# Kernel tuning notes

Measured on AMD Instinct MI355X. Metric: run time of the kernel, lower is better.

The kernel has to match this reference:

```python
import jax, jax.numpy as jnp
import numpy as np

K = 32  # neighbors per sampled point
EPS = 1e-5

def _layernorm(h, g, b):
    mu = jnp.mean(h, axis=-1, keepdims=True)
    var = jnp.mean((h - mu) ** 2, axis=-1, keepdims=True)
    return (h - mu) * jax.lax.rsqrt(var + EPS) * g + b


def setup_inputs() -> dict:
    key = jax.random.key(0)
    ks = jax.random.split(key, 20)
    N, M, D_IN, D_T = 32768, 4096, 64, 128
    s = lambda k, *sh: jax.random.normal(k, sh, dtype=jnp.float32) * 0.05
    inp = {
        "x": jax.random.normal(ks[0], (N, D_IN), dtype=jnp.float32),
        "pos": jax.random.normal(ks[1], (N, 3), dtype=jnp.float32),
        "idx": jax.random.randint(ks[2], (M,), 0, N, dtype=jnp.int32),
        "batch": jnp.zeros((N,), dtype=jnp.int32),
        # PointNetConv MLP [67 -> 128 -> 256] (ReLU after first layer only)
        "W1": s(ks[3], D_IN + 3, 128), "b1": jnp.zeros((128,), jnp.float32),
        "W2": s(ks[4], 128, 256),     "b2": jnp.zeros((256,), jnp.float32),
        # feature_reduction Linear(256, 128)
        "Wr": s(ks[5], 256, D_T), "br": jnp.zeros((D_T,), jnp.float32),
        # MultiheadAttention(128, 4)
        "in_proj_w": s(ks[6], D_T, 3 * D_T), "in_proj_b": jnp.zeros((3 * D_T,), jnp.float32),
        "out_proj_w": s(ks[7], D_T, D_T),    "out_proj_b": jnp.zeros((D_T,), jnp.float32),
        # transformer MLP [128 -> 256 -> 128]
        "Wm1": s(ks[8], D_T, 2 * D_T), "bm1": jnp.zeros((2 * D_T,), jnp.float32),
        "Wm2": s(ks[9], 2 * D_T, D_T), "bm2": jnp.zeros((D_T,), jnp.float32),
        # layer norms
        "g1": jnp.ones((D_T,), jnp.float32), "beta1": jnp.zeros((D_T,), jnp.float32),
        "g2": jnp.ones((D_T,), jnp.float32), "beta2": jnp.zeros((D_T,), jnp.float32),
    }
    return inp


def _forward(x, pos, idx, batch, W1, b1, W2, b2, Wr, br,
             in_proj_w, in_proj_b, out_proj_w, out_proj_b,
             Wm1, bm1, Wm2, bm2, g1, beta1, g2, beta2):
    q_pos = pos[idx]                                    # [M,3]
    # KNN: k nearest source points for each sampled (dst) point
    d2 = (jnp.sum(q_pos ** 2, -1, keepdims=True)
          - 2.0 * (q_pos @ pos.T)
          + jnp.sum(pos ** 2, -1)[None, :])             # [M,N]
    _, col = jax.lax.top_k(-d2, K)                      # [M,K] source indices
    # PointNetConv message: nn([x_j, pos_j - pos_i]), max-aggregate per dst
    x_j = x[col]                                        # [M,K,64]
    rel = pos[col] - q_pos[:, None, :]                  # [M,K,3]
    feat = jnp.concatenate([x_j, rel], axis=-1)         # [M,K,67]
    h = jax.nn.relu(feat @ W1 + b1) @ W2 + b2           # [M,K,256]
    agg = jnp.max(h, axis=1)                            # [M,256]
    xt = agg @ Wr + br                                  # [M,128]
    # TransformerBlock: x.view(M,1,128) -> MHA over seq len M, batch 1
    M, D = xt.shape
    H = 4
    Dh = D // H
    qkv = xt @ in_proj_w + in_proj_b                    # [M,3D]
    qh, kh, vh = [t.reshape(M, H, Dh) for t in jnp.split(qkv, 3, axis=-1)]
    scores = jnp.einsum('qhd,khd->hqk', qh, kh) / np.sqrt(Dh)
    attn = jax.nn.softmax(scores, axis=-1)
    att = jnp.einsum('hqk,khd->qhd', attn, vh).reshape(M, D)
    att = att @ out_proj_w + out_proj_b
    xt = _layernorm(xt + att, g1, beta1)
    mlp = jax.nn.relu(xt @ Wm1 + bm1) @ Wm2 + bm2
    xt = _layernorm(xt + mlp, g2, beta2)
    return xt, q_pos, batch[idx]


def reference(x, pos, idx, batch, W1, b1, W2, b2, Wr, br,
              in_proj_w, in_proj_b, out_proj_w, out_proj_b,
              Wm1, bm1, Wm2, bm2, g1, beta1, g2, beta2):
    return _forward(x, pos, idx, batch, W1, b1, W2, b2, Wr, br,
                    in_proj_w, in_proj_b, out_proj_w, out_proj_b,
                    Wm1, bm1, Wm2, bm2, g1, beta1, g2, beta2)
```

## Files before the change

kernel.cpp:

```cpp
#include <hip/hip_runtime.h>
#include <hip/hip_bf16.h>

#define DEV static __device__ __forceinline__

typedef __attribute__((ext_vector_type(8))) short          s16x8;
typedef __attribute__((ext_vector_type(8))) unsigned short u16x8;
typedef __attribute__((ext_vector_type(4))) float          f32x4;
typedef __attribute__((ext_vector_type(4))) unsigned int   u32x4;

#define MFMA16(A,B,C) __builtin_amdgcn_mfma_f32_16x16x32_bf16((A),(B),(C),0,0,0)

DEV unsigned short f2bf(float f) {
  unsigned int u = __builtin_bit_cast(unsigned int, f);
  u += 0x7fffu + ((u >> 16) & 1u);
  return (unsigned short)(u >> 16);
}

#define QSCL 0.25503562201f

#define GRID_LO  (-5.0f)
#define GRID_IH  (3.2f)

DEV int cellc(float v) {
  int c = (int)floorf((v - GRID_LO) * GRID_IH);
  return min(31, max(0, c));
}

constexpr size_t OFF_POS4  = 0;
constexpr size_t OFF_COL   = 524288;
constexpr size_t OFF_W1T   = 1048576;
constexpr size_t OFF_W2T   = OFF_W1T  + 24576;
constexpr size_t OFF_WRT   = OFF_W2T  + 65536;
constexpr size_t OFF_WQKVT = OFF_WRT  + 65536;
constexpr size_t OFF_WOUTT = OFF_WQKVT+ 98304;
constexpr size_t OFF_WM1T  = OFF_WOUTT+ 32768;
constexpr size_t OFF_WM2T  = OFF_WM1T + 65536;
constexpr size_t OFF_H     = OFF_WM2T + 65536;
constexpr size_t OFF_SPOS    = OFF_H;
constexpr size_t OFF_CELLCNT = OFF_H + 524288;
constexpr size_t OFF_CELLDSC = OFF_H + 655360;
constexpr size_t OFF_FILL    = OFF_H + 917504;
constexpr size_t OFF_PO      = OFF_H;
constexpr size_t OFF_PL      = OFF_H + 16777216;
constexpr size_t OFF_AGG   = OFF_H    + 33554432;
constexpr size_t OFF_XT0   = OFF_AGG  + 4194304;
constexpr size_t OFF_QKV   = OFF_XT0  + 2097152;
constexpr size_t OFF_ATT   = OFF_QKV  + 6291456;
constexpr size_t OFF_PRE   = OFF_ATT  + 2097152;
constexpr size_t OFF_XT1   = OFF_PRE  + 2097152;
constexpr size_t OFF_MLP1  = OFF_XT1  + 2097152;
constexpr size_t OFF_SBIAS = OFF_MLP1 + 4194304;

__global__ __launch_bounds__(256) void zero_k(int* __restrict__ p) {
  p[blockIdx.x * 256 + threadIdx.x] = 0;
}

__global__ __launch_bounds__(256) void prep_k(
    const float* __restrict__ pos, const float* __restrict__ W1,
    const float* __restrict__ W2, const float* __restrict__ Wr,
    const float* __restrict__ ipw, const float* __restrict__ ipb,
    const float* __restrict__ opw,
    const float* __restrict__ Wm1, const float* __restrict__ Wm2,
    float4* __restrict__ pos4, unsigned short* __restrict__ w1t,
    unsigned short* __restrict__ w2t, unsigned short* __restrict__ wrt,
    unsigned short* __restrict__ wqkvt, unsigned short* __restrict__ woutt,
    unsigned short* __restrict__ wm1t, unsigned short* __restrict__ wm2t,
    int* __restrict__ cellcnt, float* __restrict__ sbias) {
  int T = blockIdx.x * 256 + threadIdx.x;
  if (T < 32768) {
    float px = pos[T*3], py = pos[T*3+1], pz = pos[T*3+2];
    pos4[T] = make_float4(px, py, pz, 0.f);
    int cid = (cellc(pz)*32 + cellc(py))*32 + cellc(px);
    atomicAdd(&cellcnt[cid], 1);
    return;
  }
  T -= 32768;
  if (T < 128*96)  { int n=T/96,  k=T%96;  w1t[T]  = f2bf(k < 67 ? W1[k*128+n] : 0.f); return; }
  T -= 128*96;
  if (T < 256*128) { int n=T/128, k=T%128; w2t[T]  = f2bf(W2[k*256+n]);  return; }
  T -= 256*128;
  if (T < 128*256) { int n=T/256, k=T%256; wrt[T]  = f2bf(Wr[k*128+n]);  return; }
  T -= 128*256;
  if (T < 384*128) { int n=T/128, k=T%128;
                     float v = ipw[k*384+n];
                     if (n < 128) v *= QSCL;
                     wqkvt[T]= f2bf(v); return; }
  T -= 384*128;
  if (T < 128*128) { int n=T/128, k=T%128; woutt[T]= f2bf(opw[k*128+n]); return; }
  T -= 128*128;
  if (T < 256*128) { int n=T/128, k=T%128; wm1t[T] = f2bf(Wm1[k*256+n]); return; }
  T -= 256*128;
  if (T < 128*256) { int n=T/256, k=T%256; wm2t[T] = f2bf(Wm2[k*128+n]); return; }
  T -= 128*256;
  if (T < 384) { sbias[T] = ipb[T] * (T < 128 ? QSCL : 1.f); return; }
}

__global__ __launch_bounds__(1024) void prefix_k(const int* __restrict__ cnt,
                                                 int2* __restrict__ desc,
                                                 int* __restrict__ fill) {
  __shared__ int wsum[16];
  const int tid = threadIdx.x, lane = tid & 63, w = tid >> 6;
  int loc[32]; int s = 0;
  #pragma unroll
  for (int i = 0; i < 32; ++i) { loc[i] = cnt[tid*32 + i]; s += loc[i]; }
  int sc = s;
  #pragma unroll
  for (int off = 1; off < 64; off <<= 1) {
    int v = __shfl_up(sc, off);
    if (lane >= off) sc += v;
  }
  if (lane == 63) wsum[w] = sc;
  __syncthreads();
  if (tid == 0) {
    int run = 0;
    #pragma unroll
    for (int i = 0; i < 16; ++i) { int v = wsum[i]; wsum[i] = run; run += v; }
  }
  __syncthreads();
  int base = wsum[w] + (sc - s);
  #pragma unroll
  for (int i = 0; i < 32; ++i) {
    int c = tid*32 + i;
    desc[c] = make_int2(base, loc[i]);
    fill[c] = base;
    base += loc[i];
  }
}

__global__ __launch_bounds__(256) void scatter_k(const float4* __restrict__ pos4,
                                                 int* __restrict__ fill,
                                                 float4* __restrict__ spos) {
  int T = blockIdx.x * 256 + threadIdx.x;
  float4 p = pos4[T];
  int cid = (cellc(p.z)*32 + cellc(p.y))*32 + cellc(p.x);
  int slot = atomicAdd(&fill[cid], 1);
  spos[slot] = make_float4(p.x, p.y, p.z, __int_as_float(T));
}

#define KNN_CAP  320
#define KNN_TRIG 192
#define KNN_KEEP 33
#define KNN_INF  3e37f

__global__ __launch_bounds__(256) void knn_k(
    const float4* __restrict__ spos, const int2* __restrict__ desc,
    const float4* __restrict__ pos4, const int* __restrict__ idx,
    int* __restrict__ col,
    float* __restrict__ outqpos, float* __restrict__ outbatch) {
  __shared__ float bufd[4][KNN_CAP];
  __shared__ int   bufi[4][KNN_CAP];
  __shared__ int   shist[4][64];
  __shared__ int2  segs[4][128];
  const int tid = threadIdx.x, lane = tid & 63, w = tid >> 6;
  const unsigned long long ltmask = (1ull << lane) - 1ull;

  const int q = blockIdx.x * 4 + w;
  const int iq = idx[q];
  const float4 qp = pos4[iq];
  const float qx = qp.x, qy = qp.y, qz = qp.z;
  const int cx0 = cellc(qx), cy0 = cellc(qy), cz0 = cellc(qz);

  float t = KNN_INF;
  int cnt = 0;

  auto compact = [&]() {
    int c_ = min(cnt, KNN_CAP);
    float vd[5]; int vi[5], bs[5]; bool okv[5];
    float dmax = 1e-30f;
    #pragma unroll
    for (int s = 0; s < 5; ++s) {
      int o2 = s*64 + lane;
      okv[s] = o2 < c_;
      vd[s] = okv[s] ? bufd[w][o2] : 0.f;
      vi[s] = okv[s] ? bufi[w][o2] : 0;
      dmax = fmaxf(dmax, vd[s]);
    }
    #pragma unroll
    for (int off = 1; off < 64; off <<= 1) dmax = fmaxf(dmax, __shfl_xor(dmax, off));
    float scale = 63.99f / dmax;
    shist[w][lane] = 0;
    #pragma unroll
    for (int s = 0; s < 5; ++s) {
      bs[s] = okv[s] ? min(63, (int)(vd[s] * scale)) : 64;
      if (okv[s]) atomicAdd(&shist[w][bs[s]], 1);
    }
    int h = shist[w][lane];
    #pragma unroll
    for (int off = 1; off < 64; off <<= 1) {
      int v = __shfl_up(h, off);
      if (lane >= off) h += v;
    }
    unsigned long long mk = __ballot(h >= KNN_KEEP);
    int E = mk ? (__ffsll((long long)mk) - 1) : 63;
    int base = 0;
    #pragma unroll
    for (int s = 0; s < 5; ++s) {
      bool keep = okv[s] && bs[s] <= E;
      unsigned long long km = __ballot(keep);
      int pp = base + (int)__popcll(km & ltmask);
      if (keep) { bufd[w][pp] = vd[s]; bufi[w][pp] = vi[s]; }
      base += (int)__popcll(km);
    }
    cnt = base;
    t = fminf(t, (float)(E + 1) / scale);
  };

  auto scan_rows = [&](int knew, int kold) {
    const int S = 2*knew + 1;
    const int NR = S*S;
    const float invS = 1.f / (float)S;
    for (int r0 = 0; r0 < NR; r0 += 64) {
      int r = r0 + lane;
      bool v = r < NR;
      int dz = (int)((float)r * invS);
      int rem = r - dz*S;
      if (rem < 0) { dz--; rem += S; } else if (rem >= S) { dz++; rem -= S; }
      int ccz = cz0 + dz - knew, ccy = cy0 + rem - knew;
      bool rowok = v && ccz >= 0 && ccz < 32 && ccy >= 0 && ccy < 32;
      bool inner = kold >= 0 && abs(dz - knew) <= kold && abs(rem - knew) <= kold;
      int cbase = (ccz*32 + ccy) * 32;
      int sL = 0, lL = 0, sR = 0, lR = 0;
      if (rowok) {
        int xa = max(cx0 - knew, 0);
        int xb = inner ? (cx0 - kold - 1) : min(cx0 + knew, 31);
        if (xa <= xb) {
          int2 d0 = desc[cbase + xa];
          int2 d1 = desc[cbase + xb];
          sL = d0.x; lL = d1.x + d1.y - d0.x;
        }
        if (inner) {
          int xa2 = cx0 + kold + 1, xb2 = min(cx0 + knew, 31);
          if (xa2 <= xb2 && xa2 >= 0) {
            int2 d0 = desc[cbase + xa2];
            int2 d1 = desc[cbase + xb2];
            sR = d0.x; lR = d1.x + d1.y - d0.x;
          }
        }
      }
      int cumL = lL;
      #pragma unroll
      for (int off = 1; off < 64; off <<= 1) {
        int vv = __shfl_up(cumL, off);
        if (lane >= off) cumL += vv;
      }
      int sumL = __shfl(cumL, 63);
      int cumR = lR;
      #pragma unroll
      for (int off = 1; off < 64; off <<= 1) {
        int vv = __shfl_up(cumR, off);
        if (lane >= off) cumR += vv;
      }
      int sumR = __shfl(cumR, 63);
      segs[w][lane]      = make_int2(sL, cumL - lL);
      segs[w][64 + lane] = make_int2(sR, sumL + cumR - lR);
      const int total = sumL + sumR;

      for (int b = 0; b < total; b += 320) {
        float d2v[5]; int piv[5]; bool hv[5];
        #pragma unroll
        for (int s5 = 0; s5 < 5; ++s5) {
          int p = b + s5*64 + lane;
          bool act = p < total;
          hv[s5] = false; d2v[s5] = 0.f; piv[s5] = 0;
          if (act) {
            int lo = 0;
            #pragma unroll
            for (int st = 64; st > 0; st >>= 1)
              if (segs[w][lo + st].y <= p) lo += st;
            int2 e = segs[w][lo];
            float4 pt = spos[e.x + (p - e.y)];
            float ddx = qx-pt.x, ddy = qy-pt.y, ddz = qz-pt.z;
            float d2 = ddx*ddx + ddy*ddy + ddz*ddz;
            d2v[s5] = d2; piv[s5] = __float_as_int(pt.w);
            hv[s5] = d2 < t;
          }
        }
        #pragma unroll
        for (int s5 = 0; s5 < 5; ++s5) {
          unsigned long long hm = __ballot(hv[s5]);
          if (hm) {
            int pp = cnt + (int)__popcll(hm & ltmask);
            if (hv[s5] && pp < KNN_CAP) { bufd[w][pp] = d2v[s5]; bufi[w][pp] = piv[s5]; }
            cnt += (int)__popcll(hm);
            if (cnt >= KNN_TRIG) compact();
          }
        }
      }
    }
  };

  auto bound32 = [&]() -> float {
    int c_ = min(cnt, KNN_CAP);
    float vv[5]; bool okv[5];
    float dmax = 1e-30f;
    #pragma unroll
    for (int s = 0; s < 5; ++s) {
      int o2 = s*64 + lane;
      okv[s] = o2 < c_;
      vv[s] = okv[s] ? bufd[w][o2] : 0.f;
      dmax = fmaxf(dmax, vv[s]);
    }
    #pragma unroll
    for (int off = 1; off < 64; off <<= 1) dmax = fmaxf(dmax, __shfl_xor(dmax, off));
    float scale = 63.99f / dmax;
    shist[w][lane] = 0;
    #pragma unroll
    for (int s = 0; s < 5; ++s)
      if (okv[s]) atomicAdd(&shist[w][min(63, (int)(vv[s] * scale))], 1);
    int h = shist[w][lane];
    #pragma unroll
    for (int off = 1; off < 64; off <<= 1) {
      int v = __shfl_up(h, off);
      if (lane >= off) h += v;
    }
    unsigned long long m = __ballot(h >= 32);
    int E = m ? (__ffsll((long long)m) - 1) : 63;
    return (float)(E + 1) / scale;
  };

  int kcur = 1;
  scan_rows(1, -1);
  for (int it = 0; it < 64; ++it) {
    if (cnt >= 32) {
      float t32u = bound32();
      t = fminf(t, t32u);
      int kneed = (int)(__builtin_sqrtf(t32u) * GRID_IH) + 1;
      if (kneed <= kcur || kcur >= 31) break;
      int knew = min(kneed, 31);
      scan_rows(knew, kcur);
      kcur = knew;
    } else {
      if (kcur >= 31) break;
      int knew = min(kcur + (cnt == 0 ? 2 : 1), 31);
      scan_rows(knew, kcur);
      kcur = knew;
    }
  }

  {
    int c_ = min(cnt, KNN_CAP);
    float vd[5]; int vi[5], bs[5]; bool okf[5];
    float dmax = 1e-30f;
    #pragma unroll
    for (int s = 0; s < 5; ++s) {
      int o2 = s*64 + lane;
      okf[s] = o2 < c_;
      vd[s] = okf[s] ? bufd[w][o2] : KNN_INF;
      vi[s] = okf[s] ? bufi[w][o2] : 0;
      dmax = fmaxf(dmax, okf[s] ? vd[s] : 0.f);
    }
    #pragma unroll
    for (int off = 1; off < 64; off <<= 1) dmax = fmaxf(dmax, __shfl_xor(dmax, off));
    float sc64 = 63.99f / dmax;
    shist[w][lane] = 0;
    #pragma unroll
    for (int s = 0; s < 5; ++s) {
      bs[s] = okf[s] ? min(63, (int)(vd[s] * sc64)) : 64;
      if (okf[s]) atomicAdd(&shist[w][bs[s]], 1);
    }
    int h = shist[w][lane];
    #pragma unroll
    for (int off = 1; off < 64; off <<= 1) {
      int v = __shfl_up(h, off);
      if (lane >= off) h += v;
    }
    unsigned long long m = __ballot(h >= 32);
    int E = m ? (__ffsll((long long)m) - 1) : 63;
    int c0 = (E > 0) ? __shfl(h, E - 1) : 0;
    int base = 0;
    #pragma unroll
    for (int s = 0; s < 5; ++s) {
      bool wr = okf[s] && (bs[s] < E);
      unsigned long long km = __ballot(wr);
      int pp = base + (int)__popcll(km & ltmask);
      if (wr) col[q*32 + pp] = vi[s];
      base += (int)__popcll(km);
    }
    #pragma unroll
    for (int s = 0; s < 5; ++s)
      if (!(okf[s] && bs[s] == E)) vd[s] = KNN_INF;
    int r = 32 - c0;
    #pragma unroll 1
    for (int kk = 0; kk < r; ++kk) {
      float bd = vd[0]; int bi = vi[0]; int bc = lane*8;
      #pragma unroll
      for (int s = 1; s < 5; ++s)
        if (vd[s] < bd) { bd = vd[s]; bi = vi[s]; bc = lane*8 + s; }
      #pragma unroll
      for (int off = 1; off < 64; off <<= 1) {
        float od = __shfl_xor(bd, off);
        int   oi = __shfl_xor(bi, off);
        int   oc = __shfl_xor(bc, off);
        if (od < bd || (od == bd && oc < bc)) { bd = od; bi = oi; bc = oc; }
      }
      if ((bc >> 3) == lane) {
        int sl = bc & 7;
        #pragma unroll
        for (int s = 0; s < 5; ++s) if (sl == s) vd[s] = KNN_INF;
      }
      if (lane == 0) col[q*32 + c0 + kk] = bi;
    }
  }
  if (lane == 0) {
    outqpos[q*3+0] = qx; outqpos[q*3+1] = qy; outqpos[q*3+2] = qz;
    outbatch[q] = 0.f;
  }
}

#define LA1(r,c) S[(r)*104 + (c)]
#define LB1(r,c) S[13312 + (r)*104 + (c)]
#define HB(r,c)  S[(r)*136 + (c)]
#define W2C(r,c) S[17408 + (r)*136 + (c)]

__global__ __launch_bounds__(256) void conv_k(
    const float* __restrict__ x, const float4* __restrict__ pos4,
    const int* __restrict__ idx, const int* __restrict__ col,
    const unsigned short* __restrict__ w1t, const float* __restrict__ b1,
    const unsigned short* __restrict__ w2t, const float* __restrict__ b2,
    float* __restrict__ agg) {
  __shared__ __align__(16) unsigned short S[26624];
  __shared__ int   sci[128];
  __shared__ float sqp[4][3];
  const int tid = threadIdx.x, lane = tid & 63, w = tid >> 6;
  const int wm = w >> 1, wn = w & 1;
  const int m0 = blockIdx.x * 4;

  if (tid < 128) sci[tid] = col[m0*32 + tid];
  if (tid >= 128 && tid < 132) {
    int m = m0 + tid - 128;
    float4 p = pos4[idx[m]];
    sqp[tid-128][0] = p.x; sqp[tid-128][1] = p.y; sqp[tid-128][2] = p.z;
  }
  #pragma unroll
  for (int rnd = 0; rnd < 6; ++rnd) {
    int e = (rnd*256 + tid) * 8;
    int n = e / 96, k = e % 96;
    *(u16x8*)&LB1(n, k) = *(const u16x8*)&w1t[e];
  }
  __syncthreads();

  {
    int r = tid >> 1, half = tid & 1;
    int ci = sci[r];
    const float* src = x + (size_t)ci*64 + half*32;
    #pragma unroll
    for (int c = 0; c < 4; ++c) {
      float4 va = ((const float4*)src)[c*2], vb = ((const float4*)src)[c*2+1];
      u16x8 v;
      v[0]=f2bf(va.x); v[1]=f2bf(va.y); v[2]=f2bf(va.z); v[3]=f2bf(va.w);
      v[4]=f2bf(vb.x); v[5]=f2bf(vb.y); v[6]=f2bf(vb.z); v[7]=f2bf(vb.w);
      *(u16x8*)&LA1(r, half*32 + c*8) = v;
    }
  }
  if (tid < 128) {
    int r = tid, g = r >> 5;
    float4 p = pos4[sci[r]];
    u16x8 z;
    #pragma unroll
    for (int e = 0; e < 8; ++e) z[e] = 0;
    u16x8 v0 = z;
    v0[0] = f2bf(p.x - sqp[g][0]); v0[1] = f2bf(p.y - sqp[g][1]); v0[2] = f2bf(p.z - sqp[g][2]);
    *(u16x8*)&LA1(r, 64) = v0;
    #pragma unroll
    for (int c = 1; c < 5; ++c) *(u16x8*)&LA1(r, 64 + c*8) = z;
  }
  __syncthreads();

  f32x4 acc[4][4];
  #pragma unroll
  for (int nf = 0; nf < 4; ++nf) {
    float bv = b1[wn*64 + nf*16 + (lane & 15)];
    #pragma unroll
    for (int mf = 0; mf < 4; ++mf) acc[mf][nf] = f32x4{bv, bv, bv, bv};
  }
  #pragma unroll
  for (int kc = 0; kc < 3; ++kc) {
    s16x8 af[4], bf_[4];
    #pragma unroll
    for (int mf = 0; mf < 4; ++mf)
      af[mf] = *(const s16x8*)&LA1(wm*64 + mf*16 + (lane&15), kc*32 + (lane>>4)*8);
    #pragma unroll
    for (int nf = 0; nf < 4; ++nf)
      bf_[nf] = *(const s16x8*)&LB1(wn*64 + nf*16 + (lane&15), kc*32 + (lane>>4)*8);
    #pragma unroll
    for (int mf = 0; mf < 4; ++mf)
      #pragma unroll
      for (int nf = 0; nf < 4; ++nf)
        acc[mf][nf] = MFMA16(af[mf], bf_[nf], acc[mf][nf]);
  }
  __syncthreads();

  #pragma unroll
  for (int mf = 0; mf < 4; ++mf)
    #pragma unroll
    for (int nf = 0; nf < 4; ++nf)
      #pragma unroll
      for (int j = 0; j < 4; ++j) {
        int rloc = wm*64 + mf*16 + ((lane>>4)<<2) + j;
        int cloc = wn*64 + nf*16 + (lane & 15);
        HB(rloc, cloc) = f2bf(fmaxf(acc[mf][nf][j], 0.f));
      }
  {
    int r2 = tid >> 2, kq = (tid & 3) * 32;
    const unsigned short* src = w2t + (size_t)r2*128 + kq;
    #pragma unroll
    for (int c = 0; c < 4; ++c)
      *(u16x8*)&W2C(r2, kq + c*8) = *(const u16x8*)&src[c*8];
  }
  __syncthreads();

  #pragma unroll 1
  for (int nc = 0; nc < 4; ++nc) {
    f32x4 acc2[2][4];
    #pragma unroll
    for (int nf = 0; nf < 4; ++nf) {
      float bv = b2[nc*64 + nf*16 + (lane & 15)];
      acc2[0][nf] = f32x4{bv, bv, bv, bv};
      acc2[1][nf] = f32x4{bv, bv, bv, bv};
    }
    #pragma unroll
    for (int ks = 0; ks < 4; ++ks) {
      s16x8 af[2], bf_[4];
      #pragma unroll
      for (int mf = 0; mf < 2; ++mf)
        af[mf] = *(const s16x8*)&HB(w*32 + mf*16 + (lane&15), ks*32 + (lane>>4)*8);
      #pragma unroll
      for (int nf = 0; nf < 4; ++nf)
        bf_[nf] = *(const s16x8*)&W2C(nf*16 + (lane&15), ks*32 + (lane>>4)*8);
      #pragma unroll
      for (int mf = 0; mf < 2; ++mf)
        #pragma unroll
        for (int nf = 0; nf < 4; ++nf)
          acc2[mf][nf] = MFMA16(af[mf], bf_[nf], acc2[mf][nf]);
    }
    #pragma unroll
    for (int nf = 0; nf < 4; ++nf) {
      float mx = acc2[0][nf][0];
      #pragma unroll
      for (int j = 1; j < 4; ++j) mx = fmaxf(mx, acc2[0][nf][j]);
      #pragma unroll
      for (int j = 0; j < 4; ++j) mx = fmaxf(mx, acc2[1][nf][j]);
      mx = fmaxf(mx, __shfl_xor(mx, 16));
      mx = fmaxf(mx, __shfl_xor(mx, 32));
      if (lane < 16) agg[(size_t)(m0 + w)*256 + nc*64 + nf*16 + lane] = mx;
    }
    if (nc < 3) {
      __syncthreads();
      int r2 = tid >> 2, kq = (tid & 3) * 32;
      const unsigned short* src = w2t + (size_t)((nc+1)*64 + r2)*128 + kq;
      #pragma unroll
      for (int c = 0; c < 4; ++c)
        *(u16x8*)&W2C(r2, kq + c*8) = *(const u16x8*)&src[c*8];
      __syncthreads();
    }
  }
}

template<int KFULL, int NFULL, bool RELU, bool HAS_RES, bool OBF16>
__global__ __launch_bounds__(256) void gemm_k(
    const float* __restrict__ A, const unsigned short* __restrict__ Bt,
    const float* __restrict__ bias, const float* __restrict__ res,
    float* __restrict__ out) {
  __shared__ unsigned short lA[64][72];
  __shared__ unsigned short lB[64][72];
  const int tid = threadIdx.x, lane = tid & 63, w = tid >> 6;
  const int m0 = blockIdx.x * 64, n0 = blockIdx.y * 64;

  f32x4 acc[4];
  #pragma unroll
  for (int nf = 0; nf < 4; ++nf) {
    float bv = bias[n0 + nf*16 + (lane & 15)];
    acc[nf] = f32x4{bv, bv, bv, bv};
  }

  for (int kb = 0; kb < KFULL; kb += 64) {
    __syncthreads();
    {
      int r = tid >> 2, kq = (tid & 3) * 16;
      const float* src = A + (size_t)(m0 + r)*KFULL + kb + kq;
      #pragma unroll
      for (int c = 0; c < 2; ++c) {
        float4 va = ((const float4*)src)[c*2], vb = ((const float4*)src)[c*2+1];
        u16x8 v;
        v[0]=f2bf(va.x); v[1]=f2bf(va.y); v[2]=f2bf(va.z); v[3]=f2bf(va.w);
        v[4]=f2bf(vb.x); v[5]=f2bf(vb.y); v[6]=f2bf(vb.z); v[7]=f2bf(vb.w);
        *(u16x8*)&lA[r][kq + c*8] = v;
      }
      const unsigned short* srcb = Bt + (size_t)(n0 + r)*KFULL + kb + kq;
      #pragma unroll
      for (int c = 0; c < 2; ++c)
        *(u16x8*)&lB[r][kq + c*8] = *(const u16x8*)&srcb[c*8];
    }
    __syncthreads();
    #pragma unroll
    for (int ks = 0; ks < 2; ++ks) {
      s16x8 af = *(const s16x8*)&lA[w*16 + (lane&15)][ks*32 + (lane>>4)*8];
      s16x8 bf_[4];
      #pragma unroll
      for (int nf = 0; nf < 4; ++nf)
        bf_[nf] = *(const s16x8*)&lB[nf*16 + (lane&15)][ks*32 + (lane>>4)*8];
      #pragma unroll
      for (int nf = 0; nf < 4; ++nf)
        acc[nf] = MFMA16(af, bf_[nf], acc[nf]);
    }
  }
  #pragma unroll
  for (int nf = 0; nf < 4; ++nf)
    #pragma unroll
    for (int j = 0; j < 4; ++j) {
      int row = m0 + w*16 + ((lane>>4)<<2) + j;
      int colg = n0 + nf*16 + (lane & 15);
      float v = acc[nf][j];
      if (HAS_RES) v += res[(size_t)row*NFULL + colg];
      if (RELU)    v = fmaxf(v, 0.f);
      if (OBF16) ((unsigned short*)out)[(size_t)row*NFULL + colg] = f2bf(v);
      else       out[(size_t)row*NFULL + colg] = v;
    }
}

template<int KFULL, bool COMBINE>
__global__ __launch_bounds__(256) void gemmln_k(
    const float* __restrict__ A,
    const float* __restrict__ po, const float* __restrict__ pl,
    const unsigned short* __restrict__ Bt, const float* __restrict__ bias,
    const float* __restrict__ res,
    const float* __restrict__ gam, const float* __restrict__ bet,
    float* __restrict__ out) {
  __shared__ unsigned short lA[64][KFULL + 8];
  __shared__ unsigned short lB[128][72];
  const int tid = threadIdx.x, lane = tid & 63, w = tid >> 6;
  const int g = lane >> 4, ln_ = lane & 15;
  const int m0 = blockIdx.x * 64;

  if (COMBINE) {
    int r = tid >> 2, hh = tid & 3;
    int row = m0 + r;
    float lsum = 0.f;
    #pragma unroll
    for (int s = 0; s < 8; ++s) lsum += pl[((s*4 + hh) << 12) + row];
    float inv = 1.f / lsum;
    const float4* pob = (const float4*)po;
    #pragma unroll
    for (int c2 = 0; c2 < 4; ++c2) {
      float ax=0,ay=0,az=0,aw=0, bx=0,by=0,bz=0,bw=0;
      #pragma unroll
      for (int s = 0; s < 8; ++s) {
        size_t b = ((size_t)s*4096 + row)*32 + hh*8 + c2*2;
        float4 x0 = pob[b], x1 = pob[b+1];
        ax+=x0.x; ay+=x0.y; az+=x0.z; aw+=x0.w;
        bx+=x1.x; by+=x1.y; bz+=x1.z; bw+=x1.w;
      }
      u16x8 v;
      v[0]=f2bf(ax*inv); v[1]=f2bf(ay*inv); v[2]=f2bf(az*inv); v[3]=f2bf(aw*inv);
      v[4]=f2bf(bx*inv); v[5]=f2bf(by*inv); v[6]=f2bf(bz*inv); v[7]=f2bf(bw*inv);
      *(u16x8*)&lA[r][hh*32 + c2*8] = v;
    }
  } else {
    int r = tid >> 2, kq = (tid & 3) * (KFULL/4);
    const float* src = A + (size_t)(m0 + r)*KFULL + kq;
    #pragma unroll
    for (int c = 0; c < KFULL/32; ++c) {
      float4 va = ((const float4*)src)[c*2], vb = ((const float4*)src)[c*2+1];
      u16x8 v;
      v[0]=f2bf(va.x); v[1]=f2bf(va.y); v[2]=f2bf(va.z); v[3]=f2bf(va.w);
      v[4]=f2bf(vb.x); v[5]=f2bf(vb.y); v[6]=f2bf(vb.z); v[7]=f2bf(vb.w);
      *(u16x8*)&lA[r][kq + c*8] = v;
    }
  }

  float bv[8], gm[8], bt[8];
  #pragma unroll
  for (int nf = 0; nf < 8; ++nf) {
    bv[nf] = bias[nf*16 + ln_];
    gm[nf] = gam[nf*16 + ln_];
    bt[nf] = bet[nf*16 + ln_];
  }
  f32x4 acc[8];
  #pragma unroll
  for (int nf = 0; nf < 8; ++nf) acc[nf] = f32x4{bv[nf], bv[nf], bv[nf], bv[nf]};

  for (int kb = 0; kb < KFULL; kb += 64) {
    __syncthreads();
    {
      int r = tid >> 1, kq = (tid & 1) * 32;
      const unsigned short* src = Bt + (size_t)r*KFULL + kb + kq;
      #pragma unroll
      for (int c = 0; c < 4; ++c)
        *(u16x8*)&lB[r][kq + c*8] = *(const u16x8*)&src[c*8];
    }
    __syncthreads();
    #pragma unroll
    for (int ks = 0; ks < 2; ++ks) {
      s16x8 af = *(const s16x8*)&lA[w*16 + ln_][kb + ks*32 + g*8];
      s16x8 bf_[8];
      #pragma unroll
      for (int nf = 0; nf < 8; ++nf)
        bf_[nf] = *(const s16x8*)&lB[nf*16 + ln_][ks*32 + g*8];
      #pragma unroll
      for (int nf = 0; nf < 8; ++nf)
        acc[nf] = MFMA16(af, bf_[nf], acc[nf]);
    }
  }

  #pragma unroll
  for (int j = 0; j < 4; ++j) {
    int row = m0 + w*16 + g*4 + j;
    float sm = 0.f;
    #pragma unroll
    for (int nf = 0; nf < 8; ++nf) {
      acc[nf][j] += res[(size_t)row*128 + nf*16 + ln_];
      sm += acc[nf][j];
    }
    sm += __shfl_xor(sm, 1); sm += __shfl_xor(sm, 2);
    sm += __shfl_xor(sm, 4); sm += __shfl_xor(sm, 8);
    float mu = sm * 0.0078125f;
    float qv = 0.f;
    #pragma unroll
    for (int nf = 0; nf < 8; ++nf) {
      float d = acc[nf][j] - mu;
      qv += d*d;
    }
    qv += __shfl_xor(qv, 1); qv += __shfl_xor(qv, 2);
    qv += __shfl_xor(qv, 4); qv += __shfl_xor(qv, 8);
    float rr = rsqrtf(qv * 0.0078125f + 1e-5f);
    #pragma unroll
    for (int nf = 0; nf < 8; ++nf)
      out[(size_t)row*128 + nf*16 + ln_] = (acc[nf][j] - mu) * rr * gm[nf] + bt[nf];
  }
}

__global__ __launch_bounds__(256) void attn_k(
    const unsigned short* __restrict__ qkvb,
    float* __restrict__ po, float* __restrict__ pl) {
  __shared__ unsigned short lK[128][40];
  __shared__ unsigned short lV[32][136];
  const int tid = threadIdx.x, lane = tid & 63, w = tid >> 6;
  const int hh = blockIdx.y, sp = blockIdx.z;
  const int qr = blockIdx.x * 64 + w * 16;
  const int g = lane >> 4, q = lane & 15;

  s16x8 qf = *(const s16x8*)&qkvb[(size_t)(qr + q)*384 + hh*32 + g*8];

  f32x4 o[2];
  o[0] = f32x4{0.f,0.f,0.f,0.f}; o[1] = f32x4{0.f,0.f,0.f,0.f};
  float lrun = 0.f;

  const int srcA = q | ((2*(g & 1)) << 4);
  const int srcB = srcA + 16;
  const bool hi = (g >> 1) != 0;

  for (int kt = sp*4; kt < sp*4 + 4; ++kt) {
    const int k0 = kt * 128;
    __syncthreads();
    {
      int key = tid >> 1, d0 = (tid & 1) * 16;
      const unsigned short* src = qkvb + (size_t)(k0 + key)*384 + 128 + hh*32 + d0;
      *(u16x8*)&lK[key][d0]     = *(const u16x8*)&src[0];
      *(u16x8*)&lK[key][d0 + 8] = *(const u16x8*)&src[8];
    }
    {
      int kp = tid & 63, gg = tid >> 6;
      const unsigned short* s0 = qkvb + (size_t)(k0 + 2*kp)*384 + 256 + hh*32 + gg*8;
      u16x8 e0 = *(const u16x8*)s0;
      u16x8 e1 = *(const u16x8*)(s0 + 384);
      #pragma unroll
      for (int d = 0; d < 8; ++d) {
        unsigned int pkk = (unsigned int)e0[d] | ((unsigned int)e1[d] << 16);
        *(unsigned int*)&lV[gg*8 + d][2*kp] = pkk;
      }
    }
    __syncthreads();

    unsigned int pk[8][2];
    float ps = 0.f;
    #pragma unroll
    for (int nf = 0; nf < 8; ++nf) {
      s16x8 kf = *(const s16x8*)&lK[nf*16 + q][g*8];
      f32x4 c = MFMA16(kf, qf, (f32x4{0.f,0.f,0.f,0.f}));
      float p0 = exp2f(c[0]), p1 = exp2f(c[1]);
      float p2 = exp2f(c[2]), p3 = exp2f(c[3]);
      ps += (p0 + p1) + (p2 + p3);
      unsigned int u0 = __builtin_bit_cast(unsigned int, p0) + 0x8000u;
      unsigned int u1 = __builtin_bit_cast(unsigned int, p1) + 0x8000u;
      unsigned int u2 = __builtin_bit_cast(unsigned int, p2) + 0x8000u;
      unsigned int u3 = __builtin_bit_cast(unsigned int, p3) + 0x8000u;
      pk[nf][0] = (u0 >> 16) | (u1 & 0xffff0000u);
      pk[nf][1] = (u2 >> 16) | (u3 & 0xffff0000u);
    }
    ps += __shfl_xor(ps, 16);
    ps += __shfl_xor(ps, 32);
    lrun += ps;

    #pragma unroll
    for (int kc = 0; kc < 4; ++kc) {
      unsigned int a0 = (unsigned int)__shfl((int)pk[2*kc][0],   srcA);
      unsigned int b0 = (unsigned int)__shfl((int)pk[2*kc+1][0], srcA);
      unsigned int a1 = (unsigned int)__shfl((int)pk[2*kc][1],   srcA);
      unsigned int b1 = (unsigned int)__shfl((int)pk[2*kc+1][1], srcA);
      unsigned int a2 = (unsigned int)__shfl((int)pk[2*kc][0],   srcB);
      unsigned int b2 = (unsigned int)__shfl((int)pk[2*kc+1][0], srcB);
      unsigned int a3 = (unsigned int)__shfl((int)pk[2*kc][1],   srcB);
      unsigned int b3 = (unsigned int)__shfl((int)pk[2*kc+1][1], srcB);
      u32x4 wv;
      wv[0] = hi ? b0 : a0; wv[1] = hi ? b1 : a1;
      wv[2] = hi ? b2 : a2; wv[3] = hi ? b3 : a3;
      s16x8 pa = __builtin_bit_cast(s16x8, wv);
      #pragma unroll
      for (int df = 0; df < 2; ++df) {
        s16x8 vf = *(const s16x8*)&lV[df*16 + q][kc*32 + g*8];
        o[df] = MFMA16(pa, vf, o[df]);
      }
    }
  }
  #pragma unroll
  for (int df = 0; df < 2; ++df)
    #pragma unroll
    for (int j = 0; j < 4; ++j) {
      int row = qr + g*4 + j;
      po[((size_t)sp*4096 + row)*128 + hh*32 + df*16 + q] = o[df][j];
    }
  if (lane < 16)
    pl[((sp*4 + hh) << 12) + qr + lane] = lrun;
}

extern "C" void kernel_launch(void* const* d_in, const int* in_sizes, int n_in,
                              void* d_out, int out_size, void* d_ws, size_t ws_size,
                              hipStream_t stream) {
  const float* x    = (const float*)d_in[0];
  const float* pos  = (const float*)d_in[1];
  const int*   idx  = (const int*)d_in[2];
  const float* W1   = (const float*)d_in[4];
  const float* b1   = (const float*)d_in[5];
  const float* W2   = (const float*)d_in[6];
  const float* b2   = (const float*)d_in[7];
  const float* Wr   = (const float*)d_in[8];
  const float* br   = (const float*)d_in[9];
  const float* ipw  = (const float*)d_in[10];
  const float* ipb  = (const float*)d_in[11];
  const float* opw  = (const float*)d_in[12];
  const float* opb  = (const float*)d_in[13];
  const float* Wm1  = (const float*)d_in[14];
  const float* bm1  = (const float*)d_in[15];
  const float* Wm2  = (const float*)d_in[16];
  const float* bm2  = (const float*)d_in[17];
  const float* g1   = (const float*)d_in[18];
  const float* be1  = (const float*)d_in[19];
  const float* g2   = (const float*)d_in[20];
  const float* be2  = (const float*)d_in[21];
  float* out = (float*)d_out;
  char* ws = (char*)d_ws;

  float4*         pos4  = (float4*)(ws + OFF_POS4);
  int*            colp  = (int*)(ws + OFF_COL);
  unsigned short* w1t   = (unsigned short*)(ws + OFF_W1T);
  unsigned short* w2t   = (unsigned short*)(ws + OFF_W2T);
  unsigned short* wrt   = (unsigned short*)(ws + OFF_WRT);
  unsigned short* wqkvt = (unsigned short*)(ws + OFF_WQKVT);
  unsigned short* woutt = (unsigned short*)(ws + OFF_WOUTT);
  unsigned short* wm1t  = (unsigned short*)(ws + OFF_WM1T);
  unsigned short* wm2t  = (unsigned short*)(ws + OFF_WM2T);
  float4* sposp = (float4*)(ws + OFF_SPOS);
  int*    ccnt  = (int*)(ws + OFF_CELLCNT);
  int2*   cdesc = (int2*)(ws + OFF_CELLDSC);
  int*    cfill = (int*)(ws + OFF_FILL);
  float*  pop   = (float*)(ws + OFF_PO);
  float*  plp   = (float*)(ws + OFF_PL);
  float* aggp  = (float*)(ws + OFF_AGG);
  float* xt0p  = (float*)(ws + OFF_XT0);
  unsigned short* qkvb = (unsigned short*)(ws + OFF_QKV);
  float* xt1p  = (float*)(ws + OFF_XT1);
  float* mlp1p = (float*)(ws + OFF_MLP1);
  float* sbias = (float*)(ws + OFF_SBIAS);

  zero_k<<<128, 256, 0, stream>>>(ccnt);
  prep_k<<<946, 256, 0, stream>>>(pos, W1, W2, Wr, ipw, ipb, opw, Wm1, Wm2,
                                  pos4, w1t, w2t, wrt, wqkvt, woutt, wm1t, wm2t,
                                  ccnt, sbias);
  prefix_k<<<1, 1024, 0, stream>>>(ccnt, cdesc, cfill);
  scatter_k<<<128, 256, 0, stream>>>(pos4, cfill, sposp);
  knn_k<<<1024, 256, 0, stream>>>(sposp, cdesc, pos4, idx, colp,
                                  out + 524288, out + 536576);
  conv_k<<<1024, 256, 0, stream>>>(x, pos4, idx, colp, w1t, b1, w2t, b2, aggp);
  gemm_k<256, 128, false, false, false><<<dim3(64, 2), 256, 0, stream>>>(aggp, wrt, br, nullptr, xt0p);
  gemm_k<128, 384, false, false, true><<<dim3(64, 6), 256, 0, stream>>>(xt0p, wqkvt, sbias, nullptr, (float*)qkvb);
  attn_k<<<dim3(64, 4, 8), 256, 0, stream>>>(qkvb, pop, plp);
  gemmln_k<128, true><<<64, 256, 0, stream>>>(nullptr, pop, plp, woutt, opb, xt0p, g1, be1, xt1p);
  gemm_k<128, 256, true, false, false><<<dim3(64, 4), 256, 0, stream>>>(xt1p, wm1t, bm1, nullptr, mlp1p);
  gemmln_k<256, false><<<64, 256, 0, stream>>>(mlp1p, nullptr, nullptr, wm2t, bm2, xt1p, g2, be2, out);
}
```

Before: 168.1 us.

## Split-K the GEMM+LayerNorm kernels across warps with 16-row tiles

The fused GEMM+LayerNorm kernel now handles 16 rows per block instead of 64, so the grid grows from 64 to 256 blocks. Each of the four warps computes a quarter of the K dimension, and the partial sums are reduced through shared memory before the LayerNorm epilogue. The full weight matrix is loaded into LDS once per block rather than in K-chunks. The aim is to fill more CUs on these small launches, at the cost of more shared memory, redundant weight loads across blocks, and an extra reduction pass.

```diff
diff --git a/kernel.cpp b/kernel.cpp
--- a/kernel.cpp
+++ b/kernel.cpp
@@ -626,106 +626,110 @@
     const float* __restrict__ res,
     const float* __restrict__ gam, const float* __restrict__ bet,
     float* __restrict__ out) {
-  __shared__ unsigned short lA[64][KFULL + 8];
-  __shared__ unsigned short lB[128][72];
+  constexpr int KP = KFULL + 8;
+  __shared__ __align__(16) unsigned short lA[16 * KP];
+  __shared__ __align__(16) unsigned short lB[128 * KP];
+  __shared__ float red[4][16 * 132];
   const int tid = threadIdx.x, lane = tid & 63, w = tid >> 6;
   const int g = lane >> 4, ln_ = lane & 15;
-  const int m0 = blockIdx.x * 64;
-
-  if (COMBINE) {
-    int r = tid >> 2, hh = tid & 3;
+  const int m0 = blockIdx.x * 16;
+
+  {
+    int r = tid >> 4, seg = tid & 15;
     int row = m0 + r;
-    float lsum = 0.f;
-    #pragma unroll
-    for (int s = 0; s < 8; ++s) lsum += pl[((s*4 + hh) << 12) + row];
-    float inv = 1.f / lsum;
-    const float4* pob = (const float4*)po;
-    #pragma unroll
-    for (int c2 = 0; c2 < 4; ++c2) {
-      float ax=0,ay=0,az=0,aw=0, bx=0,by=0,bz=0,bw=0;
+    if (COMBINE) {
+      int hh = seg >> 2;
+      float lsum = 0.f;
+      #pragma unroll
+      for (int s = 0; s < 8; ++s) lsum += pl[((s*4 + hh) << 12) + row];
+      float inv = 1.f / lsum;
+      float a0=0,a1=0,a2=0,a3=0,a4=0,a5=0,a6=0,a7=0;
       #pragma unroll
       for (int s = 0; s < 8; ++s) {
-        size_t b = ((size_t)s*4096 + row)*32 + hh*8 + c2*2;
-        float4 x0 = pob[b], x1 = pob[b+1];
-        ax+=x0.x; ay+=x0.y; az+=x0.z; aw+=x0.w;
-        bx+=x1.x; by+=x1.y; bz+=x1.z; bw+=x1.w;
+        const float4* pb = (const float4*)(po + ((size_t)s*4096 + row)*128 + seg*8);
+        float4 x0 = pb[0], x1 = pb[1];
+        a0+=x0.x; a1+=x0.y; a2+=x0.z; a3+=x0.w;
+        a4+=x1.x; a5+=x1.y; a6+=x1.z; a7+=x1.w;
       }
       u16x8 v;
-      v[0]=f2bf(ax*inv); v[1]=f2bf(ay*inv); v[2]=f2bf(az*inv); v[3]=f2bf(aw*inv);
-      v[4]=f2bf(bx*inv); v[5]=f2bf(by*inv); v[6]=f2bf(bz*inv); v[7]=f2bf(bw*inv);
-      *(u16x8*)&lA[r][hh*32 + c2*8] = v;
-    }
-  } else {
-    int r = tid >> 2, kq = (tid & 3) * (KFULL/4);
-    const float* src = A + (size_t)(m0 + r)*KFULL + kq;
-    #pragma unroll
-    for (int c = 0; c < KFULL/32; ++c) {
-      float4 va = ((const float4*)src)[c*2], vb = ((const float4*)src)[c*2+1];
-      u16x8 v;
-      v[0]=f2bf(va.x); v[1]=f2bf(va.y); v[2]=f2bf(va.z); v[3]=f2bf(va.w);
-      v[4]=f2bf(vb.x); v[5]=f2bf(vb.y); v[6]=f2bf(vb.z); v[7]=f2bf(vb.w);
-      *(u16x8*)&lA[r][kq + c*8] = v;
-    }
-  }
-
-  float bv[8], gm[8], bt[8];
+      v[0]=f2bf(a0*inv); v[1]=f2bf(a1*inv); v[2]=f2bf(a2*inv); v[3]=f2bf(a3*inv);
+      v[4]=f2bf(a4*inv); v[5]=f2bf(a5*inv); v[6]=f2bf(a6*inv); v[7]=f2bf(a7*inv);
+      *(u16x8*)&lA[r*KP + seg*8] = v;
+    } else {
+      const float* src = A + (size_t)row*KFULL + seg*(KFULL/16);
+      #pragma unroll
+      for (int c = 0; c < KFULL/128; ++c) {
+        float4 va = ((const float4*)src)[c*2], vb = ((const float4*)src)[c*2+1];
+        u16x8 v;
+        v[0]=f2bf(va.x); v[1]=f2bf(va.y); v[2]=f2bf(va.z); v[3]=f2bf(va.w);
+        v[4]=f2bf(vb.x); v[5]=f2bf(vb.y); v[6]=f2bf(vb.z); v[7]=f2bf(vb.w);
+        *(u16x8*)&lA[r*KP + seg*(KFULL/16) + c*8] = v;
+      }
+    }
+  }
+  {
+    int n = tid >> 1, half = tid & 1;
+    int kb = half * (KFULL/2);
+    const unsigned short* src = Bt + (size_t)n*KFULL + kb;
+    #pragma unroll
+    for (int c = 0; c < KFULL/16; ++c)
+      *(u16x8*)&lB[n*KP + kb + c*8] = *(const u16x8*)&src[c*8];
+  }
+
+  f32x4 acc[8];
   #pragma unroll
   for (int nf = 0; nf < 8; ++nf) {
-    bv[nf] = bias[nf*16 + ln_];
-    gm[nf] = gam[nf*16 + ln_];
-    bt[nf] = bet[nf*16 + ln_];
-  }
-  f32x4 acc[8];
-  #pragma unroll
-  for (int nf = 0; nf < 8; ++nf) acc[nf] = f32x4{bv[nf], bv[nf], bv[nf], bv[nf]};
-
-  for (int kb = 0; kb < KFULL; kb += 64) {
-    __syncthreads();
-    {
-      int r = tid >> 1, kq = (tid & 1) * 32;
-      const unsigned short* src = Bt + (size_t)r*KFULL + kb + kq;
-      #pragma unroll
-      for (int c = 0; c < 4; ++c)
-        *(u16x8*)&lB[r][kq + c*8] = *(const u16x8*)&src[c*8];
-    }
-    __syncthreads();
-    #pragma unroll
-    for (int ks = 0; ks < 2; ++ks) {
-      s16x8 af = *(const s16x8*)&lA[w*16 + ln_][kb + ks*32 + g*8];
-      s16x8 bf_[8];
-      #pragma unroll
-      for (int nf = 0; nf < 8; ++nf)
-        bf_[nf] = *(const s16x8*)&lB[nf*16 + ln_][ks*32 + g*8];
-      #pragma unroll
-      for (int nf = 0; nf < 8; ++nf)
-        acc[nf] = MFMA16(af, bf_[nf], acc[nf]);
-    }
-  }
-
-  #pragma unroll
-  for (int j = 0; j < 4; ++j) {
-    int row = m0 + w*16 + g*4 + j;
-    float sm = 0.f;
+    float bv = (w == 0) ? bias[nf*16 + ln_] : 0.f;
+    acc[nf] = f32x4{bv, bv, bv, bv};
+  }
+  __syncthreads();
+
+  const int kw = w * (KFULL/4);
+  #pragma unroll
+  for (int ks = 0; ks < KFULL/128; ++ks) {
+    s16x8 af = *(const s16x8*)&lA[ln_*KP + kw + ks*32 + g*8];
+    s16x8 bf_[8];
+    #pragma unroll
+    for (int nf = 0; nf < 8; ++nf)
+      bf_[nf] = *(const s16x8*)&lB[(nf*16 + ln_)*KP + kw + ks*32 + g*8];
+    #pragma unroll
+    for (int nf = 0; nf < 8; ++nf)
+      acc[nf] = MFMA16(af, bf_[nf], acc[nf]);
+  }
+
+  #pragma unroll
+  for (int nf = 0; nf < 8; ++nf)
+    #pragma unroll
+    for (int j = 0; j < 4; ++j)
+      red[w][(g*4 + j)*132 + nf*16 + ln_] = acc[nf][j];
+  __syncthreads();
+
+  {
+    int r = tid >> 4, seg = tid & 15;
+    int row = m0 + r;
+    float v[8]; float sm = 0.f;
     #pragma unroll
     for (int nf = 0; nf < 8; ++nf) {
-      acc[nf][j] += res[(size_t)row*128 + nf*16 + ln_];
-      sm += acc[nf][j];
+      int c = nf*16 + seg;
+      float xx = red[0][r*132 + c] + red[1][r*132 + c]
+               + red[2][r*132 + c] + red[3][r*132 + c]
+               + res[(size_t)row*128 + c];
+      v[nf] = xx; sm += xx;
     }
     sm += __shfl_xor(sm, 1); sm += __shfl_xor(sm, 2);
     sm += __shfl_xor(sm, 4); sm += __shfl_xor(sm, 8);
     float mu = sm * 0.0078125f;
     float qv = 0.f;
     #pragma unroll
-    for (int nf = 0; nf < 8; ++nf) {
-      float d = acc[nf][j] - mu;
-      qv += d*d;
-    }
+    for (int nf = 0; nf < 8; ++nf) { float d = v[nf] - mu; qv += d*d; }
     qv += __shfl_xor(qv, 1); qv += __shfl_xor(qv, 2);
     qv += __shfl_xor(qv, 4); qv += __shfl_xor(qv, 8);
     float rr = rsqrtf(qv * 0.0078125f + 1e-5f);
     #pragma unroll
-    for (int nf = 0; nf < 8; ++nf)
-      out[(size_t)row*128 + nf*16 + ln_] = (acc[nf][j] - mu) * rr * gm[nf] + bt[nf];
+    for (int nf = 0; nf < 8; ++nf) {
+      int c = nf*16 + seg;
+      out[(size_t)row*128 + c] = (v[nf] - mu) * rr * gam[c] + bet[c];
+    }
   }
 }
 
@@ -884,7 +888,7 @@
   gemm_k<256, 128, false, false, false><<<dim3(64, 2), 256, 0, stream>>>(aggp, wrt, br, nullptr, xt0p);
   gemm_k<128, 384, false, false, true><<<dim3(64, 6), 256, 0, stream>>>(xt0p, wqkvt, sbias, nullptr, (float*)qkvb);
   attn_k<<<dim3(64, 4, 8), 256, 0, stream>>>(qkvb, pop, plp);
-  gemmln_k<128, true><<<64, 256, 0, stream>>>(nullptr, pop, plp, woutt, opb, xt0p, g1, be1, xt1p);
+  gemmln_k<128, true><<<256, 256, 0, stream>>>(nullptr, pop, plp, woutt, opb, xt0p, g1, be1, xt1p);
   gemm_k<128, 256, true, false, false><<<dim3(64, 4), 256, 0, stream>>>(xt1p, wm1t, bm1, nullptr, mlp1p);
-  gemmln_k<256, false><<<64, 256, 0, stream>>>(mlp1p, nullptr, nullptr, wm2t, bm2, xt1p, g2, be2, out);
-}
+  gemmln_k<256, false><<<256, 256, 0, stream>>>(mlp1p, nullptr, nullptr, wm2t, bm2, xt1p, g2, be2, out);
+}
```

Result: faster. 158.1 us (-5.9%).
